# Kernel tuning notes

Measured on AMD Instinct MI355X. Metric: run time of the kernel, lower is better.

Reference implementation:

```python
import jax, jax.numpy as jnp
import numpy as np

NUM_GROUPS = 64  # fixed for jit; indices are drawn in [0, 64)
H = 7
W = 7

def setup_inputs() -> dict:
    key = jax.random.key(0)
    k1, k2 = jax.random.split(key)
    x = jax.random.normal(k1, (2048, 512, 7, 7), dtype=jnp.float32)
    idx = jax.random.randint(k2, (2048,), 0, NUM_GROUPS, dtype=jnp.int32)
    return {"x": x, "tensor_list_assignmentindices": idx}

def reference(x, tensor_list_assignmentindices):
    # x: [N, M, H, W]; indices: [N] in [0, NUM_GROUPS)
    # Fused: sum over spatial dims first, then scatter-add per group.
    # Mathematically identical to scatter-then-spatial-sum in the original.
    x_sp = jnp.sum(x, axis=(2, 3))  # [N, M]
    group_sum = jax.ops.segment_sum(x_sp, tensor_list_assignmentindices,
                                    num_segments=NUM_GROUPS)  # [G, M]
    counts = jax.ops.segment_sum(jnp.ones((x.shape[0],), dtype=x.dtype),
                                 tensor_list_assignmentindices,
                                 num_segments=NUM_GROUPS)  # [G]
    out = group_sum / (counts[:, None] * (H * W))  # [G, M]
    return out[:, :, None, None]  # [G, M, 1, 1]
```

## Files before the change

### kernel.cpp

```cpp
#include <hip/hip_runtime.h>


#define N_SAMPLES 2048
#define M_CHANNELS 512
#define SPATIAL 49
#define GROUPS 64

__global__ __launch_bounds__(128) void spatial_scatter_kernel(
    const float* __restrict__ x, const int* __restrict__ idx,
    float* __restrict__ accum) {
  const int n = blockIdx.x;
  const int t = threadIdx.x;
  const int g = idx[n];

  const float4* p = reinterpret_cast<const float4*>(x)
                    + (size_t)n * (M_CHANNELS * SPATIAL / 4)
                    + (size_t)t * SPATIAL;

  float s0 = 0.f, s1 = 0.f, s2 = 0.f, s3 = 0.f;
#pragma unroll
  for (int j = 0; j < SPATIAL; ++j) {
    const float4 v = p[j];
#pragma unroll
    for (int k = 0; k < 4; ++k) {
      const int e = 4 * j + k;
      const int c = e / SPATIAL;
      const float val = (k == 0) ? v.x : (k == 1) ? v.y : (k == 2) ? v.z : v.w;
      if (c == 0) s0 += val;
      else if (c == 1) s1 += val;
      else if (c == 2) s2 += val;
      else s3 += val;
    }
  }

  float* a = accum + (size_t)g * M_CHANNELS + 4 * t;
  atomicAdd(a + 0, s0);
  atomicAdd(a + 1, s1);
  atomicAdd(a + 2, s2);
  atomicAdd(a + 3, s3);
}

__global__ __launch_bounds__(512) void finalize_kernel(
    const int* __restrict__ idx, float* __restrict__ out) {
  const int g = blockIdx.x;
  const int t = threadIdx.x;

  __shared__ int cnt;
  if (t == 0) cnt = 0;
  __syncthreads();

  int local = 0;
#pragma unroll
  for (int i = 0; i < N_SAMPLES / 512; ++i)
    local += (idx[t + i * 512] == g) ? 1 : 0;
  atomicAdd(&cnt, local);
  __syncthreads();

  const float inv = 1.0f / ((float)cnt * (float)SPATIAL);
  out[(size_t)g * M_CHANNELS + t] *= inv;
}

extern "C" void kernel_launch(void* const* d_in, const int* in_sizes, int n_in,
                              void* d_out, int out_size, void* d_ws, size_t ws_size,
                              hipStream_t stream) {
  const float* x = (const float*)d_in[0];
  const int* idx = (const int*)d_in[1];
  float* out = (float*)d_out;

  hipMemsetAsync(out, 0, (size_t)GROUPS * M_CHANNELS * sizeof(float), stream);

  spatial_scatter_kernel<<<N_SAMPLES, 128, 0, stream>>>(x, idx, out);
  finalize_kernel<<<GROUPS, M_CHANNELS, 0, stream>>>(idx, out);
}
```

Measured before the change: 315.7 us.

## Stage sample halves into LDS via coalesced global_load_lds before channel reduction

Each sample is split across two 256-thread blocks. Each block copies its contiguous half into shared memory with direct global-to-LDS loads, then each thread sums one channel's 49 spatial values from LDS. This replaces the old per-thread strided float4 reads, which were poorly coalesced, and issues one atomic per channel. The cost is about 50KB of LDS per block, which limits occupancy.

```diff
diff --git a/kernel.cpp b/kernel.cpp
--- a/kernel.cpp
+++ b/kernel.cpp
@@ -5,39 +5,48 @@
 #define M_CHANNELS 512
 #define SPATIAL 49
 #define GROUPS 64
+#define SAMPLE_FLOATS (M_CHANNELS * SPATIAL)
+#define HALF_FLOATS (SAMPLE_FLOATS / 2)
+#define HALF_F4 (HALF_FLOATS / 4)
 
-__global__ __launch_bounds__(128) void spatial_scatter_kernel(
+typedef __attribute__((address_space(1))) const void global_void;
+typedef __attribute__((address_space(3))) void lds_void;
+
+__global__ __launch_bounds__(256) void scatter_kernel(
     const float* __restrict__ x, const int* __restrict__ idx,
     float* __restrict__ accum) {
-  const int n = blockIdx.x;
+  __shared__ float lds[HALF_FLOATS];
+  const int blk = blockIdx.x;
+  const int n = blk >> 1;
+  const int h = blk & 1;
   const int t = threadIdx.x;
+  const int wave = t >> 6;
+  const int lane = t & 63;
   const int g = idx[n];
 
-  const float4* p = reinterpret_cast<const float4*>(x)
-                    + (size_t)n * (M_CHANNELS * SPATIAL / 4)
-                    + (size_t)t * SPATIAL;
+  const float* src = x + (size_t)n * SAMPLE_FLOATS + (size_t)h * HALF_FLOATS;
 
-  float s0 = 0.f, s1 = 0.f, s2 = 0.f, s3 = 0.f;
 #pragma unroll
-  for (int j = 0; j < SPATIAL; ++j) {
-    const float4 v = p[j];
+  for (int k = 0; k < 12; ++k) {
+    const int base_f4 = k * 256 + wave * 64;
+    __builtin_amdgcn_global_load_lds(
+        (global_void*)(src + (size_t)(base_f4 + lane) * 4),
+        (lds_void*)(lds + (size_t)base_f4 * 4), 16, 0, 0);
+  }
+  if (wave == 0) {
+    const int base_f4 = 12 * 256;
+    __builtin_amdgcn_global_load_lds(
+        (global_void*)(src + (size_t)(base_f4 + lane) * 4),
+        (lds_void*)(lds + (size_t)base_f4 * 4), 16, 0, 0);
+  }
+  __syncthreads();
+
+  const float* row = lds + t * SPATIAL;
+  float s = 0.f;
 #pragma unroll
-    for (int k = 0; k < 4; ++k) {
-      const int e = 4 * j + k;
-      const int c = e / SPATIAL;
-      const float val = (k == 0) ? v.x : (k == 1) ? v.y : (k == 2) ? v.z : v.w;
-      if (c == 0) s0 += val;
-      else if (c == 1) s1 += val;
-      else if (c == 2) s2 += val;
-      else s3 += val;
-    }
-  }
+  for (int i = 0; i < SPATIAL; ++i) s += row[i];
 
-  float* a = accum + (size_t)g * M_CHANNELS + 4 * t;
-  atomicAdd(a + 0, s0);
-  atomicAdd(a + 1, s1);
-  atomicAdd(a + 2, s2);
-  atomicAdd(a + 3, s3);
+  atomicAdd(accum + (size_t)g * M_CHANNELS + h * 256 + t, s);
 }
 
 __global__ __launch_bounds__(512) void finalize_kernel(
@@ -69,6 +78,6 @@
 
   hipMemsetAsync(out, 0, (size_t)GROUPS * M_CHANNELS * sizeof(float), stream);
 
-  spatial_scatter_kernel<<<N_SAMPLES, 128, 0, stream>>>(x, idx, out);
+  scatter_kernel<<<N_SAMPLES * 2, 256, 0, stream>>>(x, idx, out);
   finalize_kernel<<<GROUPS, M_CHANNELS, 0, stream>>>(idx, out);
 }
```

New measurement: 279.0 us. -11.6%, faster.
